# Optimization experiments

Measured on AMD Instinct MI355X. Metric: run time of the kernel, lower is better.

## Reference

```python
import jax, jax.numpy as jnp
import numpy as np

DT = 0.001  # forward-arg default in the original module
EPS = 1e-10


def setup_inputs() -> dict:
    key = jax.random.key(0)
    k1, k2 = jax.random.split(key)
    x = jax.random.normal(k1, (5000, 512, 16), dtype=jnp.float32)  # [nt, traces, channels]
    y = jax.random.normal(k2, (5000, 512, 16), dtype=jnp.float32)
    return {"x": x, "y": y}


def reference(x, y):
    # Per-(t,c) L2 norms over time axis (dim 0): shape [T, C]
    xnorm = jnp.linalg.norm(x, ord=2, axis=0) + EPS
    ynorm = jnp.linalg.norm(y, ord=2, axis=0) + EPS
    # Per-(t,c) dot products over time: shape [T, C]
    dots = jnp.einsum('ntc,ntc->tc', x, y)
    # cc = -dot(xn * dt, yn) = -dt * dot(x, y) / (||x|| * ||y||)
    cc = -DT * dots / (xnorm * ynorm)
    # Original skips slices where max|x| == 0 (contributes 0.0)
    mask = jnp.max(jnp.abs(x), axis=0) > 0
    return jnp.sum(jnp.where(mask, cc, jnp.zeros_like(cc)))
```

## Files before the change

### kernel.cpp

```cpp
#include <hip/hip_runtime.h>
#include <hip/hip_bf16.h>
#include <math.h>


#define NT_TOTAL 5000
#define NCOL     8192
#define NCOL4    2048
#define COLBLK   8

__global__ __launch_bounds__(256) void ncc_partial(const float4* __restrict__ x,
                                                   const float4* __restrict__ y,
                                                   float4* __restrict__ ws,
                                                   int clen) {
    const int col4  = blockIdx.x * 256 + threadIdx.x;
    const int ch    = blockIdx.y;
    int n0 = ch * clen;
    int n1 = n0 + clen;
    if (n1 > NT_TOTAL) n1 = NT_TOTAL;

    const float4* xp = x + (size_t)n0 * NCOL4 + col4;
    const float4* yp = y + (size_t)n0 * NCOL4 + col4;

    float4 sxx = make_float4(0.f, 0.f, 0.f, 0.f);
    float4 syy = make_float4(0.f, 0.f, 0.f, 0.f);
    float4 sxy = make_float4(0.f, 0.f, 0.f, 0.f);
    float4 mx  = make_float4(0.f, 0.f, 0.f, 0.f);

    const int steps = n1 - n0;
    #pragma unroll 4
    for (int i = 0; i < steps; ++i) {
        float4 a = xp[(size_t)i * NCOL4];
        float4 b = yp[(size_t)i * NCOL4];
        sxx.x = fmaf(a.x, a.x, sxx.x);
        sxx.y = fmaf(a.y, a.y, sxx.y);
        sxx.z = fmaf(a.z, a.z, sxx.z);
        sxx.w = fmaf(a.w, a.w, sxx.w);
        syy.x = fmaf(b.x, b.x, syy.x);
        syy.y = fmaf(b.y, b.y, syy.y);
        syy.z = fmaf(b.z, b.z, syy.z);
        syy.w = fmaf(b.w, b.w, syy.w);
        sxy.x = fmaf(a.x, b.x, sxy.x);
        sxy.y = fmaf(a.y, b.y, sxy.y);
        sxy.z = fmaf(a.z, b.z, sxy.z);
        sxy.w = fmaf(a.w, b.w, sxy.w);
        mx.x = fmaxf(mx.x, fabsf(a.x));
        mx.y = fmaxf(mx.y, fabsf(a.y));
        mx.z = fmaxf(mx.z, fabsf(a.z));
        mx.w = fmaxf(mx.w, fabsf(a.w));
    }

    const int nchunk = gridDim.y;
    float4* SXX = ws;
    float4* SYY = ws + (size_t)nchunk * NCOL4;
    float4* SXY = ws + (size_t)2 * nchunk * NCOL4;
    float4* MX  = ws + (size_t)3 * nchunk * NCOL4;
    const size_t idx = (size_t)ch * NCOL4 + col4;
    SXX[idx] = sxx;
    SYY[idx] = syy;
    SXY[idx] = sxy;
    MX[idx]  = mx;
}

__global__ __launch_bounds__(256) void ncc_combine(const float* __restrict__ ws,
                                                   float* __restrict__ partials,
                                                   int nchunk) {
    const int c = blockIdx.x * 256 + threadIdx.x;
    const float* SXX = ws;
    const float* SYY = ws + (size_t)nchunk * NCOL;
    const float* SXY = ws + (size_t)2 * nchunk * NCOL;
    const float* MX  = ws + (size_t)3 * nchunk * NCOL;

    float sxx = 0.f, syy = 0.f, sxy = 0.f, mx = 0.f;
    for (int ch = 0; ch < nchunk; ++ch) {
        const size_t idx = (size_t)ch * NCOL + c;
        sxx += SXX[idx];
        syy += SYY[idx];
        sxy += SXY[idx];
        mx = fmaxf(mx, MX[idx]);
    }

    float cc = 0.f;
    if (mx > 0.f) {
        float xn = sqrtf(sxx) + 1e-10f;
        float yn = sqrtf(syy) + 1e-10f;
        cc = -0.001f * sxy / (xn * yn);
    }

    for (int off = 32; off > 0; off >>= 1)
        cc += __shfl_down(cc, off);

    __shared__ float red[4];
    const int lane = threadIdx.x & 63;
    const int w    = threadIdx.x >> 6;
    if (lane == 0) red[w] = cc;
    __syncthreads();
    if (threadIdx.x == 0)
        partials[blockIdx.x] = red[0] + red[1] + red[2] + red[3];
}

__global__ __launch_bounds__(64) void ncc_final(const float* __restrict__ partials,
                                                float* __restrict__ out) {
    float v = (threadIdx.x < 32) ? partials[threadIdx.x] : 0.f;
    for (int off = 32; off > 0; off >>= 1)
        v += __shfl_down(v, off);
    if (threadIdx.x == 0) out[0] = v;
}

extern "C" void kernel_launch(void* const* d_in, const int* in_sizes, int n_in,
                              void* d_out, int out_size, void* d_ws, size_t ws_size,
                              hipStream_t stream) {
    const float* x = (const float*)d_in[0];
    const float* y = (const float*)d_in[1];
    float* out = (float*)d_out;
    float* ws  = (float*)d_ws;

    const size_t per_chunk_bytes = 4ull * NCOL * sizeof(float);
    size_t avail = (ws_size > 256) ? (ws_size - 256) : 0;
    int nchunk = (int)(avail / per_chunk_bytes);
    if (nchunk > 50) nchunk = 50;
    if (nchunk < 1)  nchunk = 1;
    const int clen = (NT_TOTAL + nchunk - 1) / nchunk;

    float* partials = ws + 4ull * (size_t)nchunk * NCOL;

    dim3 g1(COLBLK, nchunk);
    ncc_partial<<<g1, 256, 0, stream>>>((const float4*)x, (const float4*)y,
                                        (float4*)ws, clen);
    ncc_combine<<<32, 256, 0, stream>>>(ws, partials, nchunk);
    ncc_final<<<1, 64, 0, stream>>>(partials, out);
}
```

Before: 78.56 us.

## Switch partial reduction to scalar per-column threads and vectorize combine

The partial kernel now gives each thread one column with scalar loads instead of four columns with float4 loads. That quadruples the block count (32×nchunk blocks) and reduces per-thread register state, at the cost of narrower memory transactions. The combine kernel now reads float4 from the workspace with 64-thread blocks, each thread handling four columns. This drops the shared-memory cross-wave reduction. Narrower global loads in the bandwidth-bound main pass may lower effective bandwidth, traded against more parallelism.

```diff
diff --git a/kernel.cpp b/kernel.cpp
--- a/kernel.cpp
+++ b/kernel.cpp
@@ -5,97 +5,98 @@
 
 #define NT_TOTAL 5000
 #define NCOL     8192
-#define NCOL4    2048
-#define COLBLK   8
 
-__global__ __launch_bounds__(256) void ncc_partial(const float4* __restrict__ x,
-                                                   const float4* __restrict__ y,
-                                                   float4* __restrict__ ws,
-                                                   int clen) {
-    const int col4  = blockIdx.x * 256 + threadIdx.x;
-    const int ch    = blockIdx.y;
+__global__ __launch_bounds__(256) void ncc_partial(const float* __restrict__ x,
+                                                   const float* __restrict__ y,
+                                                   float* __restrict__ ws,
+                                                   int clen, int nchunk) {
+    const int c  = blockIdx.x * 256 + threadIdx.x;
+    const int ch = blockIdx.y;
     int n0 = ch * clen;
     int n1 = n0 + clen;
     if (n1 > NT_TOTAL) n1 = NT_TOTAL;
+    const int steps = n1 - n0;
 
-    const float4* xp = x + (size_t)n0 * NCOL4 + col4;
-    const float4* yp = y + (size_t)n0 * NCOL4 + col4;
+    const float* xp = x + (size_t)n0 * NCOL + c;
+    const float* yp = y + (size_t)n0 * NCOL + c;
 
-    float4 sxx = make_float4(0.f, 0.f, 0.f, 0.f);
-    float4 syy = make_float4(0.f, 0.f, 0.f, 0.f);
-    float4 sxy = make_float4(0.f, 0.f, 0.f, 0.f);
-    float4 mx  = make_float4(0.f, 0.f, 0.f, 0.f);
+    float sxx = 0.f, syy = 0.f, sxy = 0.f, mx = 0.f;
 
-    const int steps = n1 - n0;
-    #pragma unroll 4
-    for (int i = 0; i < steps; ++i) {
-        float4 a = xp[(size_t)i * NCOL4];
-        float4 b = yp[(size_t)i * NCOL4];
-        sxx.x = fmaf(a.x, a.x, sxx.x);
-        sxx.y = fmaf(a.y, a.y, sxx.y);
-        sxx.z = fmaf(a.z, a.z, sxx.z);
-        sxx.w = fmaf(a.w, a.w, sxx.w);
-        syy.x = fmaf(b.x, b.x, syy.x);
-        syy.y = fmaf(b.y, b.y, syy.y);
-        syy.z = fmaf(b.z, b.z, syy.z);
-        syy.w = fmaf(b.w, b.w, syy.w);
-        sxy.x = fmaf(a.x, b.x, sxy.x);
-        sxy.y = fmaf(a.y, b.y, sxy.y);
-        sxy.z = fmaf(a.z, b.z, sxy.z);
-        sxy.w = fmaf(a.w, b.w, sxy.w);
-        mx.x = fmaxf(mx.x, fabsf(a.x));
-        mx.y = fmaxf(mx.y, fabsf(a.y));
-        mx.z = fmaxf(mx.z, fabsf(a.z));
-        mx.w = fmaxf(mx.w, fabsf(a.w));
+    int i = 0;
+    for (; i + 4 <= steps; i += 4) {
+        float a0 = xp[0];
+        float a1 = xp[NCOL];
+        float a2 = xp[2 * NCOL];
+        float a3 = xp[3 * NCOL];
+        float b0 = yp[0];
+        float b1 = yp[NCOL];
+        float b2 = yp[2 * NCOL];
+        float b3 = yp[3 * NCOL];
+        xp += 4 * NCOL;
+        yp += 4 * NCOL;
+        sxx = fmaf(a0, a0, sxx); syy = fmaf(b0, b0, syy); sxy = fmaf(a0, b0, sxy);
+        mx  = fmaxf(mx, fabsf(a0));
+        sxx = fmaf(a1, a1, sxx); syy = fmaf(b1, b1, syy); sxy = fmaf(a1, b1, sxy);
+        mx  = fmaxf(mx, fabsf(a1));
+        sxx = fmaf(a2, a2, sxx); syy = fmaf(b2, b2, syy); sxy = fmaf(a2, b2, sxy);
+        mx  = fmaxf(mx, fabsf(a2));
+        sxx = fmaf(a3, a3, sxx); syy = fmaf(b3, b3, syy); sxy = fmaf(a3, b3, sxy);
+        mx  = fmaxf(mx, fabsf(a3));
+    }
+    for (; i < steps; ++i) {
+        float a = xp[0];
+        float b = yp[0];
+        xp += NCOL;
+        yp += NCOL;
+        sxx = fmaf(a, a, sxx); syy = fmaf(b, b, syy); sxy = fmaf(a, b, sxy);
+        mx  = fmaxf(mx, fabsf(a));
     }
 
-    const int nchunk = gridDim.y;
-    float4* SXX = ws;
-    float4* SYY = ws + (size_t)nchunk * NCOL4;
-    float4* SXY = ws + (size_t)2 * nchunk * NCOL4;
-    float4* MX  = ws + (size_t)3 * nchunk * NCOL4;
-    const size_t idx = (size_t)ch * NCOL4 + col4;
+    float* SXX = ws;
+    float* SYY = ws + (size_t)nchunk * NCOL;
+    float* SXY = ws + (size_t)2 * nchunk * NCOL;
+    float* MX  = ws + (size_t)3 * nchunk * NCOL;
+    const size_t idx = (size_t)ch * NCOL + c;
     SXX[idx] = sxx;
     SYY[idx] = syy;
     SXY[idx] = sxy;
     MX[idx]  = mx;
 }
 
-__global__ __launch_bounds__(256) void ncc_combine(const float* __restrict__ ws,
-                                                   float* __restrict__ partials,
-                                                   int nchunk) {
-    const int c = blockIdx.x * 256 + threadIdx.x;
-    const float* SXX = ws;
-    const float* SYY = ws + (size_t)nchunk * NCOL;
-    const float* SXY = ws + (size_t)2 * nchunk * NCOL;
-    const float* MX  = ws + (size_t)3 * nchunk * NCOL;
+__global__ __launch_bounds__(64) void ncc_combine(const float4* __restrict__ ws4,
+                                                  float* __restrict__ partials,
+                                                  int nchunk) {
+    const int c4 = blockIdx.x * 64 + threadIdx.x;
+    const int NC4 = NCOL / 4;
+    const float4* SXX = ws4;
+    const float4* SYY = ws4 + (size_t)nchunk * NC4;
+    const float4* SXY = ws4 + (size_t)2 * nchunk * NC4;
+    const float4* MX  = ws4 + (size_t)3 * nchunk * NC4;
 
-    float sxx = 0.f, syy = 0.f, sxy = 0.f, mx = 0.f;
+    float4 sxx = make_float4(0.f, 0.f, 0.f, 0.f);
+    float4 syy = make_float4(0.f, 0.f, 0.f, 0.f);
+    float4 sxy = make_float4(0.f, 0.f, 0.f, 0.f);
+    float4 mx  = make_float4(0.f, 0.f, 0.f, 0.f);
     for (int ch = 0; ch < nchunk; ++ch) {
-        const size_t idx = (size_t)ch * NCOL + c;
-        sxx += SXX[idx];
-        syy += SYY[idx];
-        sxy += SXY[idx];
-        mx = fmaxf(mx, MX[idx]);
+        const size_t idx = (size_t)ch * NC4 + c4;
+        float4 a = SXX[idx], b = SYY[idx], d = SXY[idx], m = MX[idx];
+        sxx.x += a.x; sxx.y += a.y; sxx.z += a.z; sxx.w += a.w;
+        syy.x += b.x; syy.y += b.y; syy.z += b.z; syy.w += b.w;
+        sxy.x += d.x; sxy.y += d.y; sxy.z += d.z; sxy.w += d.w;
+        mx.x = fmaxf(mx.x, m.x); mx.y = fmaxf(mx.y, m.y);
+        mx.z = fmaxf(mx.z, m.z); mx.w = fmaxf(mx.w, m.w);
     }
 
     float cc = 0.f;
-    if (mx > 0.f) {
-        float xn = sqrtf(sxx) + 1e-10f;
-        float yn = sqrtf(syy) + 1e-10f;
-        cc = -0.001f * sxy / (xn * yn);
-    }
+    if (mx.x > 0.f) cc += -0.001f * sxy.x / ((sqrtf(sxx.x) + 1e-10f) * (sqrtf(syy.x) + 1e-10f));
+    if (mx.y > 0.f) cc += -0.001f * sxy.y / ((sqrtf(sxx.y) + 1e-10f) * (sqrtf(syy.y) + 1e-10f));
+    if (mx.z > 0.f) cc += -0.001f * sxy.z / ((sqrtf(sxx.z) + 1e-10f) * (sqrtf(syy.z) + 1e-10f));
+    if (mx.w > 0.f) cc += -0.001f * sxy.w / ((sqrtf(sxx.w) + 1e-10f) * (sqrtf(syy.w) + 1e-10f));
 
     for (int off = 32; off > 0; off >>= 1)
         cc += __shfl_down(cc, off);
-
-    __shared__ float red[4];
-    const int lane = threadIdx.x & 63;
-    const int w    = threadIdx.x >> 6;
-    if (lane == 0) red[w] = cc;
-    __syncthreads();
     if (threadIdx.x == 0)
-        partials[blockIdx.x] = red[0] + red[1] + red[2] + red[3];
+        partials[blockIdx.x] = cc;
 }
 
 __global__ __launch_bounds__(64) void ncc_final(const float* __restrict__ partials,
@@ -123,9 +124,8 @@
 
     float* partials = ws + 4ull * (size_t)nchunk * NCOL;
 
-    dim3 g1(COLBLK, nchunk);
-    ncc_partial<<<g1, 256, 0, stream>>>((const float4*)x, (const float4*)y,
-                                        (float4*)ws, clen);
-    ncc_combine<<<32, 256, 0, stream>>>(ws, partials, nchunk);
+    dim3 g1(NCOL / 256, nchunk);
+    ncc_partial<<<g1, 256, 0, stream>>>(x, y, ws, clen, nchunk);
+    ncc_combine<<<32, 64, 0, stream>>>((const float4*)ws, partials, nchunk);
     ncc_final<<<1, 64, 0, stream>>>(partials, out);
 }
```

Measured after the change: 81.69 us. +4.0%, slower.
